# Kernel optimization log

Hardware: AMD Instinct MI355X
Metric: run time of the kernel (lower is better)

Reference implementation:

```python
import jax, jax.numpy as jnp
import numpy as np

NUM_CLASSES = 14  # centroids_pred has 14 centroids; target labels in [0,14)


def smooth(x):
    # smooth-L1: 0.5*x^2 if |x|<1 else |x|-0.5
    ax = jnp.abs(x)
    return jnp.where(ax < 1.0, 0.5 * x * x, ax - 0.5)


def setup_inputs() -> dict:
    key = jax.random.key(0)
    k1, k2, k3, k4, k5 = jax.random.split(key, 5)
    B, N, P = 32, 16384, 4096
    return {
        "displacement_pred": jax.random.normal(k1, (B, N), dtype=jnp.float32),
        "subsampled_points": jax.random.normal(k2, (B, 3, N), dtype=jnp.float32),
        "centroids_pred": jax.random.normal(k3, (B, 3, NUM_CLASSES), dtype=jnp.float32),
        "origin_points": jax.random.normal(k4, (B, 9, P), dtype=jnp.float32),
        "target": jax.random.randint(k5, (B, P), 0, NUM_CLASSES, dtype=jnp.int64),
    }


def reference(displacement_pred, subsampled_points, centroids_pred, origin_points, target):
    # origin_points: [B,9,P] -> xyz [B,P,3]
    xyz = jnp.transpose(origin_points, (0, 2, 1))[:, :, :3]
    # per-batch, per-class centroid means (get_centroids), vectorized via one-hot
    onehot = jax.nn.one_hot(target, NUM_CLASSES, dtype=xyz.dtype)       # [B,P,C]
    sums = jnp.einsum('bpc,bpd->bcd', onehot, xyz)                      # [B,C,3]
    counts = jnp.sum(onehot, axis=1)                                    # [B,C]
    cent_gt = sums / jnp.maximum(counts, 1.0)[:, :, None]               # [B,C,3]

    # distance estimate loss: nearest-GT-centroid distance per subsampled point
    sub = jnp.transpose(subsampled_points, (0, 2, 1))                   # [B,N,3]
    d2 = jnp.sum((sub[:, :, None, :] - cent_gt[:, None, :, :]) ** 2, -1)  # [B,N,C]
    dist = jnp.sqrt(jnp.min(d2, axis=-1))                               # [B,N]
    distance_loss = jnp.sum(smooth(displacement_pred - dist), axis=1)   # [B]

    # chamfer distance loss between predicted and GT centroids
    pred = jnp.transpose(centroids_pred, (0, 2, 1))                     # [B,Cp,3]
    D = jnp.sum((pred[:, :, None, :] - cent_gt[:, None, :, :]) ** 2, -1)  # [B,Cp,C]
    l1 = jnp.sum(jnp.min(D, axis=1), axis=-1)                           # [B]
    l2 = jnp.sum(jnp.min(D, axis=2), axis=-1)                           # [B]

    # separation loss: ratio of closest to 2nd-closest euclidean distance
    Dd = jnp.sqrt(D)                                                    # [B,Cp,C]
    closest2 = -jax.lax.top_k(-Dd, 2)[0]                                # [B,Cp,2] smallest two
    separation = jnp.sum(closest2[..., 0] / closest2[..., 1], axis=-1)  # [B]

    beta = 0.1
    return jnp.sum(distance_loss + l1 + l2 + beta * separation)
```

## Files before the change

kernel.cpp:

```cpp
#include <hip/hip_runtime.h>
#include <math.h>

#define NC 14
#define BB 32
#define NN 16384
#define PP 4096

__global__ void centroids_chamfer_kernel(const float* __restrict__ origin,
                                         const int*   __restrict__ target,
                                         const float* __restrict__ cpred,
                                         float* __restrict__ cent_ws,
                                         float* __restrict__ out) {
    const int b    = blockIdx.x;
    const int tid  = threadIdx.x;
    const int lane = tid & 63;
    const int wave = tid >> 6;

    float sx[NC], sy[NC], sz[NC], sc[NC];
    #pragma unroll
    for (int c = 0; c < NC; ++c) { sx[c] = sy[c] = sz[c] = sc[c] = 0.f; }

    const float* ob = origin + (size_t)b * 9 * PP;
    const int*   tb = target + (size_t)b * PP;

    for (int p = tid; p < PP; p += 256) {
        int   t = tb[p];
        float x = ob[p], y = ob[PP + p], z = ob[2 * PP + p];
        #pragma unroll
        for (int c = 0; c < NC; ++c) {
            float m = (t == c) ? 1.f : 0.f;
            sx[c] = fmaf(m, x, sx[c]);
            sy[c] = fmaf(m, y, sy[c]);
            sz[c] = fmaf(m, z, sz[c]);
            sc[c] += m;
        }
    }

    #pragma unroll
    for (int c = 0; c < NC; ++c) {
        #pragma unroll
        for (int o = 32; o > 0; o >>= 1) {
            sx[c] += __shfl_down(sx[c], o);
            sy[c] += __shfl_down(sy[c], o);
            sz[c] += __shfl_down(sz[c], o);
            sc[c] += __shfl_down(sc[c], o);
        }
    }

    __shared__ float s_part[4][NC][4];
    if (lane == 0) {
        #pragma unroll
        for (int c = 0; c < NC; ++c) {
            s_part[wave][c][0] = sx[c];
            s_part[wave][c][1] = sy[c];
            s_part[wave][c][2] = sz[c];
            s_part[wave][c][3] = sc[c];
        }
    }
    __syncthreads();

    __shared__ float s_cent[NC][3];
    if (tid < NC * 3) {
        int c = tid / 3, d = tid % 3;
        float s = s_part[0][c][d] + s_part[1][c][d] + s_part[2][c][d] + s_part[3][c][d];
        float n = s_part[0][c][3] + s_part[1][c][3] + s_part[2][c][3] + s_part[3][c][3];
        float v = s / fmaxf(n, 1.f);
        s_cent[c][d] = v;
        cent_ws[(size_t)b * NC * 3 + tid] = v;
    }
    __syncthreads();

    __shared__ float s_D[NC][NC];
    if (tid < NC * NC) {
        int cp = tid / NC, c = tid % NC;
        float dx = cpred[(size_t)b * 3 * NC + 0 * NC + cp] - s_cent[c][0];
        float dy = cpred[(size_t)b * 3 * NC + 1 * NC + cp] - s_cent[c][1];
        float dz = cpred[(size_t)b * 3 * NC + 2 * NC + cp] - s_cent[c][2];
        s_D[cp][c] = dx * dx + dy * dy + dz * dz;
    }
    __syncthreads();

    __shared__ float s_loss;
    if (tid == 0) s_loss = 0.f;
    __syncthreads();

    if (tid < NC) {
        float mn = s_D[0][tid];
        #pragma unroll
        for (int cp = 1; cp < NC; ++cp) mn = fminf(mn, s_D[cp][tid]);

        float m1 = 1e30f, m2 = 1e30f;
        #pragma unroll
        for (int c = 0; c < NC; ++c) {
            float d = sqrtf(s_D[tid][c]);
            if (d < m1) { m2 = m1; m1 = d; }
            else if (d < m2) { m2 = d; }
        }
        float contrib = mn + m1 * m1 + 0.1f * (m1 / m2);
        atomicAdd(&s_loss, contrib);
    }
    __syncthreads();
    if (tid == 0) atomicAdd(out, s_loss);
}

__global__ void distance_loss_kernel(const float* __restrict__ disp,
                                     const float* __restrict__ sub,
                                     const float* __restrict__ cent,
                                     float* __restrict__ out) {
    const int blocksPerBatch = NN / 1024;
    const int b  = blockIdx.x / blocksPerBatch;
    const int n0 = (blockIdx.x % blocksPerBatch) * 1024 + threadIdx.x * 4;

    __shared__ float s_cent[NC * 3];
    if (threadIdx.x < NC * 3)
        s_cent[threadIdx.x] = cent[(size_t)b * NC * 3 + threadIdx.x];
    __syncthreads();

    const float4 xv = *(const float4*)&sub[((size_t)b * 3 + 0) * NN + n0];
    const float4 yv = *(const float4*)&sub[((size_t)b * 3 + 1) * NN + n0];
    const float4 zv = *(const float4*)&sub[((size_t)b * 3 + 2) * NN + n0];
    const float4 dv = *(const float4*)&disp[(size_t)b * NN + n0];

    const float xs[4] = {xv.x, xv.y, xv.z, xv.w};
    const float ys[4] = {yv.x, yv.y, yv.z, yv.w};
    const float zs[4] = {zv.x, zv.y, zv.z, zv.w};
    const float ds[4] = {dv.x, dv.y, dv.z, dv.w};

    float sm = 0.f;
    #pragma unroll
    for (int k = 0; k < 4; ++k) {
        float mn = 1e30f;
        #pragma unroll
        for (int c = 0; c < NC; ++c) {
            float dx = xs[k] - s_cent[c * 3 + 0];
            float dy = ys[k] - s_cent[c * 3 + 1];
            float dz = zs[k] - s_cent[c * 3 + 2];
            mn = fminf(mn, dx * dx + dy * dy + dz * dz);
        }
        float v  = ds[k] - sqrtf(mn);
        float av = fabsf(v);
        sm += (av < 1.f) ? 0.5f * v * v : (av - 0.5f);
    }

    #pragma unroll
    for (int o = 32; o > 0; o >>= 1) sm += __shfl_down(sm, o);

    __shared__ float s_part[4];
    const int wave = threadIdx.x >> 6;
    if ((threadIdx.x & 63) == 0) s_part[wave] = sm;
    __syncthreads();
    if (threadIdx.x == 0)
        atomicAdd(out, s_part[0] + s_part[1] + s_part[2] + s_part[3]);
}

extern "C" void kernel_launch(void* const* d_in, const int* in_sizes, int n_in,
                              void* d_out, int out_size, void* d_ws, size_t ws_size,
                              hipStream_t stream) {
    const float* disp   = (const float*)d_in[0];
    const float* sub    = (const float*)d_in[1];
    const float* cpred  = (const float*)d_in[2];
    const float* origin = (const float*)d_in[3];
    const int*   target = (const int*)d_in[4];

    float* out     = (float*)d_out;
    float* cent_ws = (float*)d_ws;

    hipMemsetAsync(out, 0, sizeof(float), stream);
    centroids_chamfer_kernel<<<BB, 256, 0, stream>>>(origin, target, cpred, cent_ws, out);
    distance_loss_kernel<<<BB * (NN / 1024), 256, 0, stream>>>(disp, sub, cent_ws, out);
}
```

Before: 93.20 us.

## Drop memset launch, use last-block reduction and vectorize centroid loads

Removes the hipMemsetAsync launch by resetting a completion counter inside the first kernel and having the last finishing block of the distance kernel sum per-block partials from workspace and write the output directly. Per-batch chamfer terms are stored to workspace instead of being atomically added to the output. The centroid accumulation loop is changed to use int4/float4 vector loads with a fixed unrolled trip count. This saves one launch and the global float atomics, at the cost of a threadfence and counter atomic per block and a serial final reduction in one block.

```diff
diff --git a/kernel.cpp b/kernel.cpp
--- a/kernel.cpp
+++ b/kernel.cpp
@@ -6,16 +6,23 @@
 #define NN 16384
 #define PP 4096
 
+#define WS_COUNTER 0
+#define WS_CHAMFER 16
+#define WS_DIST    64
+#define WS_CENT    640
+#define NBLK_B     (BB * (NN / 1024))
+
 __global__ void centroids_chamfer_kernel(const float* __restrict__ origin,
                                          const int*   __restrict__ target,
                                          const float* __restrict__ cpred,
-                                         float* __restrict__ cent_ws,
-                                         float* __restrict__ out) {
+                                         float* __restrict__ ws) {
     const int b    = blockIdx.x;
     const int tid  = threadIdx.x;
     const int lane = tid & 63;
     const int wave = tid >> 6;
 
+    if (b == 0 && tid == 0) ((unsigned int*)ws)[WS_COUNTER] = 0u;
+
     float sx[NC], sy[NC], sz[NC], sc[NC];
     #pragma unroll
     for (int c = 0; c < NC; ++c) { sx[c] = sy[c] = sz[c] = sc[c] = 0.f; }
@@ -23,16 +30,28 @@
     const float* ob = origin + (size_t)b * 9 * PP;
     const int*   tb = target + (size_t)b * PP;
 
-    for (int p = tid; p < PP; p += 256) {
-        int   t = tb[p];
-        float x = ob[p], y = ob[PP + p], z = ob[2 * PP + p];
-        #pragma unroll
-        for (int c = 0; c < NC; ++c) {
-            float m = (t == c) ? 1.f : 0.f;
-            sx[c] = fmaf(m, x, sx[c]);
-            sy[c] = fmaf(m, y, sy[c]);
-            sz[c] = fmaf(m, z, sz[c]);
-            sc[c] += m;
+    const int p0 = tid * 4;
+    #pragma unroll
+    for (int it = 0; it < PP / 1024; ++it) {
+        const int p = p0 + it * 1024;
+        const int4   tv = *(const int4*)&tb[p];
+        const float4 xv = *(const float4*)&ob[p];
+        const float4 yv = *(const float4*)&ob[PP + p];
+        const float4 zv = *(const float4*)&ob[2 * PP + p];
+        const int   ts[4] = {tv.x, tv.y, tv.z, tv.w};
+        const float xs[4] = {xv.x, xv.y, xv.z, xv.w};
+        const float ys[4] = {yv.x, yv.y, yv.z, yv.w};
+        const float zs[4] = {zv.x, zv.y, zv.z, zv.w};
+        #pragma unroll
+        for (int k = 0; k < 4; ++k) {
+            #pragma unroll
+            for (int c = 0; c < NC; ++c) {
+                float m = (ts[k] == c) ? 1.f : 0.f;
+                sx[c] = fmaf(m, xs[k], sx[c]);
+                sy[c] = fmaf(m, ys[k], sy[c]);
+                sz[c] = fmaf(m, zs[k], sz[c]);
+                sc[c] += m;
+            }
         }
     }
 
@@ -66,7 +85,7 @@
         float n = s_part[0][c][3] + s_part[1][c][3] + s_part[2][c][3] + s_part[3][c][3];
         float v = s / fmaxf(n, 1.f);
         s_cent[c][d] = v;
-        cent_ws[(size_t)b * NC * 3 + tid] = v;
+        ws[WS_CENT + (size_t)b * NC * 3 + tid] = v;
     }
     __syncthreads();
 
@@ -80,10 +99,7 @@
     }
     __syncthreads();
 
-    __shared__ float s_loss;
-    if (tid == 0) s_loss = 0.f;
-    __syncthreads();
-
+    __shared__ float s_contrib[NC];
     if (tid < NC) {
         float mn = s_D[0][tid];
         #pragma unroll
@@ -96,16 +112,20 @@
             if (d < m1) { m2 = m1; m1 = d; }
             else if (d < m2) { m2 = d; }
         }
-        float contrib = mn + m1 * m1 + 0.1f * (m1 / m2);
-        atomicAdd(&s_loss, contrib);
-    }
-    __syncthreads();
-    if (tid == 0) atomicAdd(out, s_loss);
+        s_contrib[tid] = mn + m1 * m1 + 0.1f * (m1 / m2);
+    }
+    __syncthreads();
+    if (tid == 0) {
+        float s = 0.f;
+        #pragma unroll
+        for (int c = 0; c < NC; ++c) s += s_contrib[c];
+        ws[WS_CHAMFER + b] = s;
+    }
 }
 
 __global__ void distance_loss_kernel(const float* __restrict__ disp,
                                      const float* __restrict__ sub,
-                                     const float* __restrict__ cent,
+                                     float* __restrict__ ws,
                                      float* __restrict__ out) {
     const int blocksPerBatch = NN / 1024;
     const int b  = blockIdx.x / blocksPerBatch;
@@ -113,7 +133,7 @@
 
     __shared__ float s_cent[NC * 3];
     if (threadIdx.x < NC * 3)
-        s_cent[threadIdx.x] = cent[(size_t)b * NC * 3 + threadIdx.x];
+        s_cent[threadIdx.x] = ws[WS_CENT + (size_t)b * NC * 3 + threadIdx.x];
     __syncthreads();
 
     const float4 xv = *(const float4*)&sub[((size_t)b * 3 + 0) * NN + n0];
@@ -149,8 +169,32 @@
     const int wave = threadIdx.x >> 6;
     if ((threadIdx.x & 63) == 0) s_part[wave] = sm;
     __syncthreads();
-    if (threadIdx.x == 0)
-        atomicAdd(out, s_part[0] + s_part[1] + s_part[2] + s_part[3]);
+
+    __shared__ unsigned int s_old;
+    if (threadIdx.x == 0) {
+        ws[WS_DIST + blockIdx.x] = s_part[0] + s_part[1] + s_part[2] + s_part[3];
+        __threadfence();
+        s_old = atomicAdd((unsigned int*)ws + WS_COUNTER, 1u);
+    }
+    __syncthreads();
+
+    if (s_old == NBLK_B - 1) {
+        __threadfence();
+        float acc = 0.f;
+        for (int i = threadIdx.x; i < NBLK_B; i += 256)
+            acc += __hip_atomic_load(&ws[WS_DIST + i], __ATOMIC_RELAXED,
+                                     __HIP_MEMORY_SCOPE_AGENT);
+        if (threadIdx.x < BB)
+            acc += __hip_atomic_load(&ws[WS_CHAMFER + threadIdx.x], __ATOMIC_RELAXED,
+                                     __HIP_MEMORY_SCOPE_AGENT);
+        #pragma unroll
+        for (int o = 32; o > 0; o >>= 1) acc += __shfl_down(acc, o);
+        __shared__ float s_fin[4];
+        if ((threadIdx.x & 63) == 0) s_fin[threadIdx.x >> 6] = acc;
+        __syncthreads();
+        if (threadIdx.x == 0)
+            *out = s_fin[0] + s_fin[1] + s_fin[2] + s_fin[3];
+    }
 }
 
 extern "C" void kernel_launch(void* const* d_in, const int* in_sizes, int n_in,
@@ -162,10 +206,9 @@
     const float* origin = (const float*)d_in[3];
     const int*   target = (const int*)d_in[4];
 
-    float* out     = (float*)d_out;
-    float* cent_ws = (float*)d_ws;
-
-    hipMemsetAsync(out, 0, sizeof(float), stream);
-    centroids_chamfer_kernel<<<BB, 256, 0, stream>>>(origin, target, cpred, cent_ws, out);
-    distance_loss_kernel<<<BB * (NN / 1024), 256, 0, stream>>>(disp, sub, cent_ws, out);
+    float* out = (float*)d_out;
+    float* ws  = (float*)d_ws;
+
+    centroids_chamfer_kernel<<<BB, 256, 0, stream>>>(origin, target, cpred, ws);
+    distance_loss_kernel<<<NBLK_B, 256, 0, stream>>>(disp, sub, ws, out);
 }
```

Result: slower. 135.0 us (+44.9%).
